# Performance work log

Measured on AMD Instinct MI355X. Metric: run time of the kernel, lower is better.

Reference implementation:

```python
import jax, jax.numpy as jnp
import numpy as np

DIM = 96
HEADS = 3
WIN = 7
HID = 384  # dim * mlp_ratio
EPS = 1e-5


def layernorm(x, w, b):
    mu = jnp.mean(x, axis=-1, keepdims=True)
    var = jnp.mean((x - mu) ** 2, axis=-1, keepdims=True)
    return (x - mu) * jax.lax.rsqrt(var + EPS) * w + b


def setup_inputs() -> dict:
    key = jax.random.key(0)
    ks = jax.random.split(key, 8)
    s = lambda n: 1.0 / np.sqrt(n)
    return {
        "x": jax.random.normal(ks[0], (8, DIM, 224, 224), dtype=jnp.float32),
        "norm1_w": jnp.ones((DIM,), jnp.float32),
        "norm1_b": jnp.zeros((DIM,), jnp.float32),
        "qkv_w": jax.random.normal(ks[1], (DIM, 3 * DIM), jnp.float32) * s(DIM),
        "qkv_b": jnp.zeros((3 * DIM,), jnp.float32),
        "proj_w": jax.random.normal(ks[2], (DIM, DIM), jnp.float32) * s(DIM),
        "proj_b": jnp.zeros((DIM,), jnp.float32),
        "norm2_w": jnp.ones((DIM,), jnp.float32),
        "norm2_b": jnp.zeros((DIM,), jnp.float32),
        "fc1_w": jax.random.normal(ks[3], (DIM, HID), jnp.float32) * s(DIM),
        "fc1_b": jnp.zeros((HID,), jnp.float32),
        "fc2_w": jax.random.normal(ks[4], (HID, DIM), jnp.float32) * s(HID),
        "fc2_b": jnp.zeros((DIM,), jnp.float32),
    }


def swin_block(x, norm1_w, norm1_b, qkv_w, qkv_b, proj_w, proj_b,
               norm2_w, norm2_b, fc1_w, fc1_b, fc2_w, fc2_b):
    B, C, H, W = x.shape
    hd = C // HEADS
    scale = hd ** -0.5
    N = WIN * WIN
    # [B, H*W, C]
    tok = jnp.transpose(x.reshape(B, C, H * W), (0, 2, 1))
    shortcut = tok
    t = layernorm(tok, norm1_w, norm1_b).reshape(B, H, W, C)
    nH, nW = H // WIN, W // WIN
    wins = t.reshape(B, nH, WIN, nW, WIN, C).transpose(0, 1, 3, 2, 4, 5)
    wins = wins.reshape(-1, N, C)  # [B*nH*nW, N, C]
    # window MHA
    qkv = (wins @ qkv_w + qkv_b).reshape(-1, N, 3, HEADS, hd)
    q, k, v = jnp.moveaxis(qkv, 2, 0)  # each [Bw, N, HEADS, hd]
    attn = jnp.einsum('bnhd,bmhd->bhnm', q, k) * scale
    attn = jax.nn.softmax(attn, axis=-1)
    o = jnp.einsum('bhnm,bmhd->bnhd', attn, v).reshape(-1, N, C)
    o = o @ proj_w + proj_b
    # window reverse
    o = o.reshape(B, nH, nW, WIN, WIN, C).transpose(0, 1, 3, 2, 4, 5)
    o = o.reshape(B, H * W, C)
    t = shortcut + o
    # MLP block
    m = layernorm(t, norm2_w, norm2_b)
    m = jax.nn.gelu(m @ fc1_w + fc1_b, approximate=False) @ fc2_w + fc2_b
    t = t + m
    return jnp.transpose(t, (0, 2, 1)).reshape(B, C, H, W)


def reference(x, norm1_w, norm1_b, qkv_w, qkv_b, proj_w, proj_b,
              norm2_w, norm2_b, fc1_w, fc1_b, fc2_w, fc2_b):
    return swin_block(x, norm1_w, norm1_b, qkv_w, qkv_b, proj_w, proj_b,
                      norm2_w, norm2_b, fc1_w, fc1_b, fc2_w, fc2_b)
```

## Files before the change

### kernel.cpp

```cpp
#include <hip/hip_runtime.h>


typedef __bf16 bf16;
typedef __attribute__((ext_vector_type(8))) __bf16 bf16x8;
typedef __attribute__((ext_vector_type(4))) float f32x4;
typedef __attribute__((ext_vector_type(4))) int i32x4;

#define LDA 104
#define LDV 72
#define LDW 233
#define TOKW 6144

union U8 { int i[4]; bf16x8 v; };

__device__ __forceinline__ f32x4 mfma16(bf16x8 a, bf16x8 b, f32x4 c) {
    return __builtin_amdgcn_mfma_f32_16x16x32_bf16(a, b, c, 0, 0, 0);
}
__device__ __forceinline__ int pkbf(float lo, float hi) {
    int r; asm("v_cvt_pk_bf16_f32 %0, %1, %2" : "=v"(r) : "v"(lo), "v"(hi)); return r;
}
__device__ __forceinline__ float rcpf(float x) {
    float r; asm("v_rcp_f32 %0, %1" : "=v"(r) : "v"(x)); return r;
}
__device__ __forceinline__ float gelu_f(float v) {
    const float a = -2.30220770f, b = -0.10294852f;
    float e = exp2f(v * __builtin_fmaf(b, v * v, a));
    return v * rcpf(1.f + e);
}

__global__ void swin_wprep(const float* __restrict__ qkv_w,
                           const float* __restrict__ proj_w,
                           const float* __restrict__ fc1_w,
                           const float* __restrict__ fc2_w,
                           bf16* __restrict__ wsT) {
    int i = blockIdx.x * 256 + threadIdx.x;
    if (i < 27648) { int n = i / 96, k = i - n * 96; wsT[i] = (bf16)qkv_w[k * 288 + n]; }
    else if (i < 36864) { int j = i - 27648, n = j / 96, k = j - n * 96; wsT[i] = (bf16)proj_w[k * 96 + n]; }
    else if (i < 73728) { int j = i - 36864, n = j / 96, k = j - n * 96; wsT[i] = (bf16)fc1_w[k * 384 + n]; }
    else if (i < 110592){ int j = i - 73728, n = j / 384, k = j - n * 384; wsT[i] = (bf16)fc2_w[k * 96 + n]; }
}

__global__ void swin_padfill(bf16* __restrict__ tokW) {
    int id = blockIdx.x * 256 + threadIdx.x;
    int win = id / 180, r = id - win * 180;
    int row = 49 + r / 12, c8 = r - (r / 12) * 12;
    *(i32x4*)(tokW + (size_t)win * TOKW + row * 96 + c8 * 8) = i32x4{0, 0, 0, 0};
}

__global__ __launch_bounds__(256)
void swin_gather(const float* __restrict__ x, bf16* __restrict__ tokW) {
    __shared__ bf16 sT[96 * LDW];
    const int tid = threadIdx.x;
    const int bi = blockIdx.x;
    const int b = bi / 224, h = bi - b * 224;
    const int wy = h / 7, ty = h - wy * 7;
    const size_t xbase = (size_t)b * 4816896 + (size_t)h * 224;

#pragma unroll
    for (int i = 0; i < 21; ++i) {
        int id = i * 256 + tid;
        int c = id / 56, w4 = id - c * 56;
        f32x4 v = *(const f32x4*)(x + xbase + (size_t)c * 50176 + w4 * 4);
#pragma unroll
        for (int j = 0; j < 4; ++j) sT[c * LDW + w4 * 4 + j] = (bf16)v[j];
    }
    __syncthreads();

#pragma unroll
    for (int i = 0; i < 11; ++i) {
        int id = i * 256 + tid;
        if (id < 2688) {
            int win = id / 84, r = id - win * 84;
            int tx = r / 12, c8 = r - tx * 12;
            bf16x8 v;
#pragma unroll
            for (int j = 0; j < 8; ++j) v[j] = sT[(c8 * 8 + j) * LDW + win * 7 + tx];
            *(i32x4*)(tokW + (size_t)(b * 1024 + wy * 32 + win) * TOKW
                      + (ty * 7 + tx) * 96 + c8 * 8) = *(i32x4*)&v;
        }
    }
}

__global__ __launch_bounds__(256)
void swin_scatter(const bf16* __restrict__ tokW, float* __restrict__ out) {
    __shared__ bf16 sT[96 * LDW];
    const int tid = threadIdx.x;
    const int bi = blockIdx.x;
    const int b = bi / 224, h = bi - b * 224;
    const int wy = h / 7, ty = h - wy * 7;
    const size_t obase = (size_t)b * 4816896 + (size_t)h * 224;

#pragma unroll
    for (int i = 0; i < 11; ++i) {
        int id = i * 256 + tid;
        if (id < 2688) {
            int win = id / 84, r = id - win * 84;
            int tx = r / 12, c8 = r - tx * 12;
            bf16x8 v = *(const bf16x8*)(tokW + (size_t)(b * 1024 + wy * 32 + win) * TOKW
                                        + (ty * 7 + tx) * 96 + c8 * 8);
#pragma unroll
            for (int j = 0; j < 8; ++j) sT[(c8 * 8 + j) * LDW + win * 7 + tx] = v[j];
        }
    }
    __syncthreads();

#pragma unroll
    for (int i = 0; i < 21; ++i) {
        int id = i * 256 + tid;
        int c = id / 56, w4 = id - c * 56;
        f32x4 v;
#pragma unroll
        for (int j = 0; j < 4; ++j) v[j] = (float)sT[c * LDW + w4 * 4 + j];
        *(f32x4*)(out + obase + (size_t)c * 50176 + w4 * 4) = v;
    }
}

__device__ __forceinline__ bf16x8 bload(const bf16* T, const float* worig,
                                        int nrow, int k0, int K, int N, bool wok) {
    if (wok) return *(const bf16x8*)(T + (size_t)nrow * K + k0);
    bf16x8 f;
#pragma unroll
    for (int j = 0; j < 8; ++j) f[j] = (bf16)worig[(size_t)(k0 + j) * N + nrow];
    return f;
}

__global__ __launch_bounds__(256, 4)
void swin_fused(const float* __restrict__ x, bf16* __restrict__ tokW,
                const float* __restrict__ n1w, const float* __restrict__ n1b,
                const float* __restrict__ qkvw, const float* __restrict__ qkvb,
                const float* __restrict__ projw, const float* __restrict__ projb,
                const float* __restrict__ n2w, const float* __restrict__ n2b,
                const float* __restrict__ fc1w, const float* __restrict__ fc1b,
                const float* __restrict__ fc2w, const float* __restrict__ fc2b,
                const bf16* __restrict__ wsT,
                float* __restrict__ out, int fast_i, int wok_i) {
    __shared__ __attribute__((aligned(16))) bf16 L[20224];
    bf16* RB = L;
    bf16* RC = L + 6656;
    bf16* RV = L + 13312;

    const bool fast = fast_i != 0;
    const bool wok  = wok_i != 0;

    const int tid  = threadIdx.x;
    const int wave = tid >> 6;
    const int lane = tid & 63;
    const int g    = lane >> 4;
    const int q16  = lane & 15;

    const int win = blockIdx.x;
    const int b  = win >> 10;
    const int wy = (win >> 5) & 31;
    const int wx = win & 31;
    const int h0 = wy * 7, w0 = wx * 7;
    const size_t xbase = (size_t)b * 4816896;
    const bf16* myWin = tokW + (size_t)win * TOKW;

    if (fast) {
#pragma unroll
        for (int i = 0; i < 3; ++i) {
            int id = i * 256 + tid;
            int row = id / 12, c8 = id - row * 12;
            *(i32x4*)&RB[row * LDA + c8 * 8] = *(const i32x4*)(myWin + row * 96 + c8 * 8);
        }
    } else {
        for (int i = 0; i < 24; ++i) {
            int id = i * 256 + tid;
            if (id < 4704) {
                int c = id / 49, pix = id - c * 49;
                int ty = pix / 7, tx = pix - ty * 7;
                RB[pix * LDA + c] =
                    (bf16)x[xbase + (size_t)c * 50176 + (h0 + ty) * 224 + w0 + tx];
            } else if (id < 6144) {
                int j = id - 4704;
                int row = 49 + j / 96, c = j - (j / 96) * 96;
                RB[row * LDA + c] = (bf16)0.f;
            }
        }
    }
    __syncthreads();

    {
        int r = tid >> 2, p = tid & 3;
        const int c0 = p * 24;
        bf16* rp = &RB[r * LDA + c0];
        bf16x8 v0 = *(const bf16x8*)rp;
        bf16x8 v1 = *(const bf16x8*)(rp + 8);
        bf16x8 v2 = *(const bf16x8*)(rp + 16);
        float s = 0.f, s2 = 0.f;
#pragma unroll
        for (int j = 0; j < 8; ++j) {
            float a = (float)v0[j], c = (float)v1[j], d = (float)v2[j];
            s += a + c + d; s2 += a * a + c * c + d * d;
        }
        s += __shfl_xor(s, 1);  s2 += __shfl_xor(s2, 1);
        s += __shfl_xor(s, 2);  s2 += __shfl_xor(s2, 2);
        float mu = s * (1.f / 96.f);
        float rs = rsqrtf(fmaxf(s2 * (1.f / 96.f) - mu * mu, 0.f) + 1e-5f);
        bf16x8 o0, o1, o2;
#pragma unroll
        for (int j = 0; j < 8; ++j) {
            o0[j] = (bf16)(((float)v0[j] - mu) * rs * n1w[c0 + j] + n1b[c0 + j]);
            o1[j] = (bf16)(((float)v1[j] - mu) * rs * n1w[c0 + 8 + j] + n1b[c0 + 8 + j]);
            o2[j] = (bf16)(((float)v2[j] - mu) * rs * n1w[c0 + 16 + j] + n1b[c0 + 16 + j]);
        }
        *(bf16x8*)rp = o0; *(bf16x8*)(rp + 8) = o1; *(bf16x8*)(rp + 16) = o2;
    }
    __syncthreads();

    bf16x8 afrag[3][4];
#pragma unroll
    for (int s = 0; s < 3; ++s)
#pragma unroll
        for (int m = 0; m < 4; ++m)
            afrag[s][m] = *(const bf16x8*)&RB[(m * 16 + q16) * LDA + s * 32 + g * 8];
    __syncthreads();

    const bf16* qkvT  = wsT;
    const bf16* projT = wsT + 27648;
    const bf16* fc1T  = wsT + 36864;
    const bf16* fc2T  = wsT + 73728;

    for (int nt = wave; nt < 18; nt += 4) {
        const int nrow = nt * 16 + q16;
        f32x4 acc[4] = {{0,0,0,0},{0,0,0,0},{0,0,0,0},{0,0,0,0}};
#pragma unroll
        for (int s = 0; s < 3; ++s) {
            bf16x8 bf = bload(qkvT, qkvw, nrow, s * 32 + g * 8, 96, 288, wok);
#pragma unroll
            for (int m = 0; m < 4; ++m) acc[m] = mfma16(afrag[s][m], bf, acc[m]);
        }
        float bias = qkvb[nrow];
#pragma unroll
        for (int m = 0; m < 4; ++m)
#pragma unroll
            for (int r = 0; r < 4; ++r) {
                float v = acc[m][r] + bias;
                int row = m * 16 + g * 4 + r;
                bf16 hv = (bf16)v;
                if (nrow < 96)        RB[row * LDA + nrow] = hv;
                else if (nrow < 192)  RC[row * LDA + (nrow - 96)] = hv;
                else                  RV[(nrow - 192) * LDV + row] = hv;
            }
    }
    __syncthreads();

    const float sc_l2e = 0.17677669529663688f * 1.4426950408889634f;
    const bool hi5 = (lane & 32) != 0;
    const int addr0 = ((lane & 16) << 3) | (q16 << 2);
    const int addr1 = addr0 + 64;
    f32x4 oacc[3][2];
#pragma unroll
    for (int h = 0; h < 3; ++h) {
        bf16x8 bq = *(const bf16x8*)&RB[(wave * 16 + q16) * LDA + h * 32 + g * 8];
        f32x4 s4s[4];
#pragma unroll
        for (int kt = 0; kt < 4; ++kt) {
            bf16x8 ak = *(const bf16x8*)&RC[(kt * 16 + q16) * LDA + h * 32 + g * 8];
            f32x4 z = {0, 0, 0, 0};
            s4s[kt] = mfma16(ak, bq, z);
        }
        float m0 = -1e30f;
#pragma unroll
        for (int kt = 0; kt < 3; ++kt)
#pragma unroll
            for (int r = 0; r < 4; ++r) m0 = fmaxf(m0, s4s[kt][r]);
        m0 = fmaxf(m0, (g == 0) ? s4s[3][0] : -1e30f);
        m0 = fmaxf(m0, __shfl_xor(m0, 16));
        m0 = fmaxf(m0, __shfl_xor(m0, 32));
        float ss = 0.f;
#pragma unroll
        for (int kt = 0; kt < 3; ++kt)
#pragma unroll
            for (int r = 0; r < 4; ++r) {
                float e = exp2f((s4s[kt][r] - m0) * sc_l2e);
                s4s[kt][r] = e; ss += e;
            }
        {
            float e = (g == 0) ? exp2f((s4s[3][0] - m0) * sc_l2e) : 0.f;
            s4s[3][0] = e; ss += e;
            s4s[3][1] = 0.f; s4s[3][2] = 0.f; s4s[3][3] = 0.f;
        }
        ss += __shfl_xor(ss, 16);
        ss += __shfl_xor(ss, 32);
        float inv = rcpf(ss);

        int u[4][2];
#pragma unroll
        for (int kt = 0; kt < 4; ++kt) {
            u[kt][0] = pkbf(s4s[kt][0], s4s[kt][1]);
            u[kt][1] = pkbf(s4s[kt][2], s4s[kt][3]);
        }
        bf16x8 ap[2];
#pragma unroll
        for (int kh = 0; kh < 2; ++kh) {
            U8 w;
            int a0 = __builtin_amdgcn_ds_bpermute(addr0, u[kh * 2][0]);
            int b0 = __builtin_amdgcn_ds_bpermute(addr0, u[kh * 2 + 1][0]);
            w.i[0] = hi5 ? b0 : a0;
            int a1 = __builtin_amdgcn_ds_bpermute(addr0, u[kh * 2][1]);
            int b1 = __builtin_amdgcn_ds_bpermute(addr0, u[kh * 2 + 1][1]);
            w.i[1] = hi5 ? b1 : a1;
            int a2 = __builtin_amdgcn_ds_bpermute(addr1, u[kh * 2][0]);
            int b2 = __builtin_amdgcn_ds_bpermute(addr1, u[kh * 2 + 1][0]);
            w.i[2] = hi5 ? b2 : a2;
            int a3 = __builtin_amdgcn_ds_bpermute(addr1, u[kh * 2][1]);
            int b3 = __builtin_amdgcn_ds_bpermute(addr1, u[kh * 2 + 1][1]);
            w.i[3] = hi5 ? b3 : a3;
            ap[kh] = w.v;
        }
#pragma unroll
        for (int n2 = 0; n2 < 2; ++n2) {
            int d0 = (h * 32 + n2 * 16 + q16) * LDV;
            f32x4 oa = {0, 0, 0, 0};
            oa = mfma16(*(const bf16x8*)&RV[d0 + g * 8], ap[0], oa);
            oa = mfma16(*(const bf16x8*)&RV[d0 + 32 + g * 8], ap[1], oa);
#pragma unroll
            for (int r = 0; r < 4; ++r) oa[r] *= inv;
            oacc[h][n2] = oa;
        }
    }
    __syncthreads();

    {
        int u2[3][2][2];
#pragma unroll
        for (int h = 0; h < 3; ++h)
#pragma unroll
            for (int n2 = 0; n2 < 2; ++n2) {
                u2[h][n2][0] = pkbf(oacc[h][n2][0], oacc[h][n2][1]);
                u2[h][n2][1] = pkbf(oacc[h][n2][2], oacc[h][n2][3]);
            }
        bf16x8 aoM[3];
#pragma unroll
        for (int s = 0; s < 3; ++s) {
            U8 w;
            int a0 = __builtin_amdgcn_ds_bpermute(addr0, u2[s][0][0]);
            int b0 = __builtin_amdgcn_ds_bpermute(addr0, u2[s][1][0]);
            w.i[0] = hi5 ? b0 : a0;
            int a1 = __builtin_amdgcn_ds_bpermute(addr0, u2[s][0][1]);
            int b1 = __builtin_amdgcn_ds_bpermute(addr0, u2[s][1][1]);
            w.i[1] = hi5 ? b1 : a1;
            int a2 = __builtin_amdgcn_ds_bpermute(addr1, u2[s][0][0]);
            int b2 = __builtin_amdgcn_ds_bpermute(addr1, u2[s][1][0]);
            w.i[2] = hi5 ? b2 : a2;
            int a3 = __builtin_amdgcn_ds_bpermute(addr1, u2[s][0][1]);
            int b3 = __builtin_amdgcn_ds_bpermute(addr1, u2[s][1][1]);
            w.i[3] = hi5 ? b3 : a3;
            aoM[s] = w.v;
        }
#pragma unroll
        for (int nt = 0; nt < 6; ++nt) {
            int nrow = nt * 16 + q16;
            f32x4 pacc = {0, 0, 0, 0};
#pragma unroll
            for (int s = 0; s < 3; ++s) {
                bf16x8 bf = bload(projT, projw, nrow, s * 32 + g * 8, 96, 96, wok);
                pacc = mfma16(aoM[s], bf, pacc);
            }
            float bias = projb[nrow];
#pragma unroll
            for (int r = 0; r < 4; ++r) {
                int row = wave * 16 + g * 4 + r;
                float sc;
                if (fast) sc = (float)myWin[row * 96 + nrow];
                else      sc = (row < 49)
                    ? x[xbase + (size_t)nrow * 50176 + (h0 + row / 7) * 224 + w0 + row % 7]
                    : 0.f;
                RV[row * LDA + nrow] = (bf16)(pacc[r] + bias + sc);
            }
        }
    }
    __syncthreads();

    {
        int r = tid >> 2, p = tid & 3;
        const int c0 = p * 24;
        const bf16* rp = &RV[r * LDA + c0];
        bf16x8 v0 = *(const bf16x8*)rp;
        bf16x8 v1 = *(const bf16x8*)(rp + 8);
        bf16x8 v2 = *(const bf16x8*)(rp + 16);
        float s = 0.f, s2 = 0.f;
#pragma unroll
        for (int j = 0; j < 8; ++j) {
            float a = (float)v0[j], c = (float)v1[j], d = (float)v2[j];
            s += a + c + d; s2 += a * a + c * c + d * d;
        }
        s += __shfl_xor(s, 1);  s2 += __shfl_xor(s2, 1);
        s += __shfl_xor(s, 2);  s2 += __shfl_xor(s2, 2);
        float mu = s * (1.f / 96.f);
        float rs = rsqrtf(fmaxf(s2 * (1.f / 96.f) - mu * mu, 0.f) + 1e-5f);
        bf16x8 o0, o1, o2;
#pragma unroll
        for (int j = 0; j < 8; ++j) {
            o0[j] = (bf16)(((float)v0[j] - mu) * rs * n2w[c0 + j] + n2b[c0 + j]);
            o1[j] = (bf16)(((float)v1[j] - mu) * rs * n2w[c0 + 8 + j] + n2b[c0 + 8 + j]);
            o2[j] = (bf16)(((float)v2[j] - mu) * rs * n2w[c0 + 16 + j] + n2b[c0 + 16 + j]);
        }
        bf16* wp = &RB[r * LDA + c0];
        *(bf16x8*)wp = o0; *(bf16x8*)(wp + 8) = o1; *(bf16x8*)(wp + 16) = o2;
    }
    __syncthreads();

    const int npt = (wave < 2) ? 2 : 1;
    f32x4 f2acc[2][4] = {{{0,0,0,0},{0,0,0,0},{0,0,0,0},{0,0,0,0}},
                         {{0,0,0,0},{0,0,0,0},{0,0,0,0},{0,0,0,0}}};
    for (int ch = 0; ch < 4; ++ch) {
#pragma unroll
        for (int t = 0; t < 2; ++t) {
            if (t < npt) {
                int ntl = (t == 0) ? wave : wave + 4;
                int nrow = (ch * 6 + ntl) * 16 + q16;
                f32x4 acc[4] = {{0,0,0,0},{0,0,0,0},{0,0,0,0},{0,0,0,0}};
#pragma unroll
                for (int s = 0; s < 3; ++s) {
                    bf16x8 bf = bload(fc1T, fc1w, nrow, s * 32 + g * 8, 96, 384, wok);
#pragma unroll
                    for (int m = 0; m < 4; ++m) {
                        bf16x8 a = *(const bf16x8*)&RB[(m * 16 + q16) * LDA + s * 32 + g * 8];
                        acc[m] = mfma16(a, bf, acc[m]);
                    }
                }
                float bias = fc1b[nrow];
#pragma unroll
                for (int m = 0; m < 4; ++m)
#pragma unroll
                    for (int r = 0; r < 4; ++r)
                        RC[(m * 16 + g * 4 + r) * LDA + ntl * 16 + q16] =
                            (bf16)gelu_f(acc[m][r] + bias);
            }
        }
        __syncthreads();
#pragma unroll
        for (int s = 0; s < 3; ++s) {
            bf16x8 a0 = *(const bf16x8*)&RC[(q16)      * LDA + s * 32 + g * 8];
            bf16x8 a1 = *(const bf16x8*)&RC[(16 + q16) * LDA + s * 32 + g * 8];
            bf16x8 a2 = *(const bf16x8*)&RC[(32 + q16) * LDA + s * 32 + g * 8];
            bf16x8 a3 = *(const bf16x8*)&RC[(48 + q16) * LDA + s * 32 + g * 8];
#pragma unroll
            for (int t = 0; t < 2; ++t) {
                if (t < npt) {
                    int nt = (t == 0) ? wave : wave + 4;
                    int nrow = nt * 16 + q16;
                    bf16x8 bf = bload(fc2T, fc2w, nrow, ch * 96 + s * 32 + g * 8, 384, 96, wok);
                    f2acc[t][0] = mfma16(a0, bf, f2acc[t][0]);
                    f2acc[t][1] = mfma16(a1, bf, f2acc[t][1]);
                    f2acc[t][2] = mfma16(a2, bf, f2acc[t][2]);
                    f2acc[t][3] = mfma16(a3, bf, f2acc[t][3]);
                }
            }
        }
        __syncthreads();
    }

#pragma unroll
    for (int t = 0; t < 2; ++t) {
        if (t < npt) {
            int col = ((t == 0) ? wave : wave + 4) * 16 + q16;
            float bias = fc2b[col];
#pragma unroll
            for (int m = 0; m < 4; ++m)
#pragma unroll
                for (int r = 0; r < 4; ++r) {
                    int row = m * 16 + g * 4 + r;
                    float t2 = (float)RV[row * LDA + col];
                    RV[row * LDA + col] = (bf16)(f2acc[t][m][r] + bias + t2);
                }
        }
    }
    __syncthreads();

    if (fast) {
#pragma unroll
        for (int i = 0; i < 3; ++i) {
            int id = i * 256 + tid;
            if (id < 588) {
                int row = id / 12, c8 = id - row * 12;
                *(i32x4*)(tokW + (size_t)win * TOKW + row * 96 + c8 * 8) =
                    *(const i32x4*)&RV[row * LDA + c8 * 8];
            }
        }
    } else {
        for (int i = 0; i < 19; ++i) {
            int id = i * 256 + tid;
            if (id < 4704) {
                int c = id / 49, pix = id - c * 49;
                int ty = pix / 7, tx = pix - ty * 7;
                out[xbase + (size_t)c * 50176 + (h0 + ty) * 224 + w0 + tx] =
                    (float)RV[pix * LDA + c];
            }
        }
    }
}

extern "C" void kernel_launch(void* const* d_in, const int* in_sizes, int n_in,
                              void* d_out, int out_size, void* d_ws, size_t ws_size,
                              hipStream_t stream) {
    const float* x      = (const float*)d_in[0];
    const float* n1w    = (const float*)d_in[1];
    const float* n1b    = (const float*)d_in[2];
    const float* qkv_w  = (const float*)d_in[3];
    const float* qkv_b  = (const float*)d_in[4];
    const float* proj_w = (const float*)d_in[5];
    const float* proj_b = (const float*)d_in[6];
    const float* n2w    = (const float*)d_in[7];
    const float* n2b    = (const float*)d_in[8];
    const float* fc1_w  = (const float*)d_in[9];
    const float* fc1_b  = (const float*)d_in[10];
    const float* fc2_w  = (const float*)d_in[11];
    const float* fc2_b  = (const float*)d_in[12];
    float* out = (float*)d_out;

    const size_t TOKW_OFF = 225280;
    const int wok  = (ws_size >= 221184) ? 1 : 0;
    const int fast = (ws_size >= TOKW_OFF + 100663296ull) ? 1 : 0;
    bf16* wsT  = (bf16*)d_ws;
    bf16* tokW = (bf16*)((char*)d_ws + TOKW_OFF);

    if (wok)
        swin_wprep<<<dim3(432), dim3(256), 0, stream>>>(qkv_w, proj_w, fc1_w, fc2_w, wsT);
    if (fast) {
        swin_padfill<<<dim3(5760), dim3(256), 0, stream>>>(tokW);
        swin_gather<<<dim3(1792), dim3(256), 0, stream>>>(x, tokW);
    }
    swin_fused<<<dim3(8192), dim3(256), 0, stream>>>(
        x, tokW, n1w, n1b, qkv_w, qkv_b, proj_w, proj_b, n2w, n2b,
        fc1_w, fc1_b, fc2_w, fc2_b, wsT, out, fast, wok);
    if (fast)
        swin_scatter<<<dim3(1792), dim3(256), 0, stream>>>(tokW, out);
}
```

Before: 444.5 us.

## Keep per-wave token rows in registers through proj, LayerNorm2 and MLP

Result: slower. 785.1 us (+76.6%).

```diff
diff --git a/kernel.cpp b/kernel.cpp
--- a/kernel.cpp
+++ b/kernel.cpp
@@ -26,6 +26,29 @@
     const float a = -2.30220770f, b = -0.10294852f;
     float e = exp2f(v * __builtin_fmaf(b, v * v, a));
     return v * rcpf(1.f + e);
+}
+__device__ __forceinline__ float bf2f(int dw, int hi) {
+    union { int i; float f; } u;
+    u.i = hi ? (dw & 0xffff0000) : (dw << 16);
+    return u.f;
+}
+
+__device__ __forceinline__ bf16x8 xp(int p0, int p1, int q0, int q1,
+                                     int addr0, int addr1, bool hi5) {
+    U8 w;
+    int a0 = __builtin_amdgcn_ds_bpermute(addr0, p0);
+    int b0 = __builtin_amdgcn_ds_bpermute(addr0, q0);
+    w.i[0] = hi5 ? b0 : a0;
+    int a1 = __builtin_amdgcn_ds_bpermute(addr0, p1);
+    int b1 = __builtin_amdgcn_ds_bpermute(addr0, q1);
+    w.i[1] = hi5 ? b1 : a1;
+    int a2 = __builtin_amdgcn_ds_bpermute(addr1, p0);
+    int b2 = __builtin_amdgcn_ds_bpermute(addr1, q0);
+    w.i[2] = hi5 ? b2 : a2;
+    int a3 = __builtin_amdgcn_ds_bpermute(addr1, p1);
+    int b3 = __builtin_amdgcn_ds_bpermute(addr1, q1);
+    w.i[3] = hi5 ? b3 : a3;
+    return w.v;
 }
 
 __global__ void swin_wprep(const float* __restrict__ qkv_w,
@@ -134,10 +157,9 @@
                 const float* __restrict__ fc2w, const float* __restrict__ fc2b,
                 const bf16* __restrict__ wsT,
                 float* __restrict__ out, int fast_i, int wok_i) {
-    __shared__ __attribute__((aligned(16))) bf16 L[20224];
+    __shared__ __attribute__((aligned(16))) bf16 L[13568];
     bf16* RB = L;
-    bf16* RC = L + 6656;
-    bf16* RV = L + 13312;
+    bf16* RV = L + 6656;
 
     const bool fast = fast_i != 0;
     const bool wok  = wok_i != 0;
@@ -155,6 +177,10 @@
     const int h0 = wy * 7, w0 = wx * 7;
     const size_t xbase = (size_t)b * 4816896;
     const bf16* myWin = tokW + (size_t)win * TOKW;
+
+    const bool hi5 = (lane & 32) != 0;
+    const int addr0 = ((lane & 16) << 3) | (q16 << 2);
+    const int addr1 = addr0 + 64;
 
     if (fast) {
 #pragma unroll
@@ -221,44 +247,69 @@
     const bf16* fc1T  = wsT + 36864;
     const bf16* fc2T  = wsT + 73728;
 
-    for (int nt = wave; nt < 18; nt += 4) {
-        const int nrow = nt * 16 + q16;
-        f32x4 acc[4] = {{0,0,0,0},{0,0,0,0},{0,0,0,0},{0,0,0,0}};
-#pragma unroll
-        for (int s = 0; s < 3; ++s) {
-            bf16x8 bf = bload(qkvT, qkvw, nrow, s * 32 + g * 8, 96, 288, wok);
-#pragma unroll
-            for (int m = 0; m < 4; ++m) acc[m] = mfma16(afrag[s][m], bf, acc[m]);
-        }
-        float bias = qkvb[nrow];
-#pragma unroll
-        for (int m = 0; m < 4; ++m)
-#pragma unroll
-            for (int r = 0; r < 4; ++r) {
-                float v = acc[m][r] + bias;
-                int row = m * 16 + g * 4 + r;
-                bf16 hv = (bf16)v;
-                if (nrow < 96)        RB[row * LDA + nrow] = hv;
-                else if (nrow < 192)  RC[row * LDA + (nrow - 96)] = hv;
-                else                  RV[(nrow - 192) * LDV + row] = hv;
-            }
+    bf16x8 bq[3];
+    {
+        int uq[6][2];
+#pragma unroll
+        for (int nt = 0; nt < 6; ++nt) {
+            f32x4 qa = {0, 0, 0, 0};
+#pragma unroll
+            for (int s = 0; s < 3; ++s)
+                qa = mfma16(bload(qkvT, qkvw, nt * 16 + q16, s * 32 + g * 8, 96, 288, wok),
+                            afrag[s][wave], qa);
+            f32x4 qb = *(const f32x4*)(qkvb + nt * 16 + g * 4);
+            uq[nt][0] = pkbf(qa[0] + qb[0], qa[1] + qb[1]);
+            uq[nt][1] = pkbf(qa[2] + qb[2], qa[3] + qb[3]);
+        }
+#pragma unroll
+        for (int h = 0; h < 3; ++h)
+            bq[h] = xp(uq[2 * h][0], uq[2 * h][1], uq[2 * h + 1][0], uq[2 * h + 1][1],
+                       addr0, addr1, hi5);
+    }
+
+    {
+        const int base = 6 + wave * 3;
+#pragma unroll
+        for (int i = 0; i < 3; ++i) {
+            const int nt = base + i;
+            const int nrow = nt * 16 + q16;
+            f32x4 acc[4] = {{0,0,0,0},{0,0,0,0},{0,0,0,0},{0,0,0,0}};
+#pragma unroll
+            for (int s = 0; s < 3; ++s) {
+                bf16x8 bf = bload(qkvT, qkvw, nrow, s * 32 + g * 8, 96, 288, wok);
+#pragma unroll
+                for (int m = 0; m < 4; ++m) acc[m] = mfma16(afrag[s][m], bf, acc[m]);
+            }
+            float bias = qkvb[nrow];
+            if (wave < 2) {
+#pragma unroll
+                for (int m = 0; m < 4; ++m)
+#pragma unroll
+                    for (int r = 0; r < 4; ++r)
+                        RB[(m * 16 + g * 4 + r) * LDA + (nt - 6) * 16 + q16] =
+                            (bf16)(acc[m][r] + bias);
+            } else {
+#pragma unroll
+                for (int m = 0; m < 4; ++m)
+#pragma unroll
+                    for (int r = 0; r < 4; ++r)
+                        RV[((nt - 12) * 16 + q16) * LDV + m * 16 + g * 4 + r] =
+                            (bf16)(acc[m][r] + bias);
+            }
+        }
     }
     __syncthreads();
 
     const float sc_l2e = 0.17677669529663688f * 1.4426950408889634f;
-    const bool hi5 = (lane & 32) != 0;
-    const int addr0 = ((lane & 16) << 3) | (q16 << 2);
-    const int addr1 = addr0 + 64;
     f32x4 oacc[3][2];
 #pragma unroll
     for (int h = 0; h < 3; ++h) {
-        bf16x8 bq = *(const bf16x8*)&RB[(wave * 16 + q16) * LDA + h * 32 + g * 8];
         f32x4 s4s[4];
 #pragma unroll
         for (int kt = 0; kt < 4; ++kt) {
-            bf16x8 ak = *(const bf16x8*)&RC[(kt * 16 + q16) * LDA + h * 32 + g * 8];
+            bf16x8 ak = *(const bf16x8*)&RB[(kt * 16 + q16) * LDA + h * 32 + g * 8];
             f32x4 z = {0, 0, 0, 0};
-            s4s[kt] = mfma16(ak, bq, z);
+            s4s[kt] = mfma16(ak, bq[h], z);
         }
         float m0 = -1e30f;
 #pragma unroll
@@ -291,181 +342,128 @@
             u[kt][0] = pkbf(s4s[kt][0], s4s[kt][1]);
             u[kt][1] = pkbf(s4s[kt][2], s4s[kt][3]);
         }
-        bf16x8 ap[2];
-#pragma unroll
-        for (int kh = 0; kh < 2; ++kh) {
-            U8 w;
-            int a0 = __builtin_amdgcn_ds_bpermute(addr0, u[kh * 2][0]);
-            int b0 = __builtin_amdgcn_ds_bpermute(addr0, u[kh * 2 + 1][0]);
-            w.i[0] = hi5 ? b0 : a0;
-            int a1 = __builtin_amdgcn_ds_bpermute(addr0, u[kh * 2][1]);
-            int b1 = __builtin_amdgcn_ds_bpermute(addr0, u[kh * 2 + 1][1]);
-            w.i[1] = hi5 ? b1 : a1;
-            int a2 = __builtin_amdgcn_ds_bpermute(addr1, u[kh * 2][0]);
-            int b2 = __builtin_amdgcn_ds_bpermute(addr1, u[kh * 2 + 1][0]);
-            w.i[2] = hi5 ? b2 : a2;
-            int a3 = __builtin_amdgcn_ds_bpermute(addr1, u[kh * 2][1]);
-            int b3 = __builtin_amdgcn_ds_bpermute(addr1, u[kh * 2 + 1][1]);
-            w.i[3] = hi5 ? b3 : a3;
-            ap[kh] = w.v;
-        }
+        bf16x8 ap0 = xp(u[0][0], u[0][1], u[1][0], u[1][1], addr0, addr1, hi5);
+        bf16x8 ap1 = xp(u[2][0], u[2][1], u[3][0], u[3][1], addr0, addr1, hi5);
 #pragma unroll
         for (int n2 = 0; n2 < 2; ++n2) {
             int d0 = (h * 32 + n2 * 16 + q16) * LDV;
             f32x4 oa = {0, 0, 0, 0};
-            oa = mfma16(*(const bf16x8*)&RV[d0 + g * 8], ap[0], oa);
-            oa = mfma16(*(const bf16x8*)&RV[d0 + 32 + g * 8], ap[1], oa);
+            oa = mfma16(*(const bf16x8*)&RV[d0 + g * 8], ap0, oa);
+            oa = mfma16(*(const bf16x8*)&RV[d0 + 32 + g * 8], ap1, oa);
 #pragma unroll
             for (int r = 0; r < 4; ++r) oa[r] *= inv;
             oacc[h][n2] = oa;
         }
     }
-    __syncthreads();
-
+
+    float t2f[6][4];
     {
-        int u2[3][2][2];
+        int uo[3][2][2];
 #pragma unroll
         for (int h = 0; h < 3; ++h)
 #pragma unroll
             for (int n2 = 0; n2 < 2; ++n2) {
-                u2[h][n2][0] = pkbf(oacc[h][n2][0], oacc[h][n2][1]);
-                u2[h][n2][1] = pkbf(oacc[h][n2][2], oacc[h][n2][3]);
+                uo[h][n2][0] = pkbf(oacc[h][n2][0], oacc[h][n2][1]);
+                uo[h][n2][1] = pkbf(oacc[h][n2][2], oacc[h][n2][3]);
             }
         bf16x8 aoM[3];
 #pragma unroll
-        for (int s = 0; s < 3; ++s) {
-            U8 w;
-            int a0 = __builtin_amdgcn_ds_bpermute(addr0, u2[s][0][0]);
-            int b0 = __builtin_amdgcn_ds_bpermute(addr0, u2[s][1][0]);
-            w.i[0] = hi5 ? b0 : a0;
-            int a1 = __builtin_amdgcn_ds_bpermute(addr0, u2[s][0][1]);
-            int b1 = __builtin_amdgcn_ds_bpermute(addr0, u2[s][1][1]);
-            w.i[1] = hi5 ? b1 : a1;
-            int a2 = __builtin_amdgcn_ds_bpermute(addr1, u2[s][0][0]);
-            int b2 = __builtin_amdgcn_ds_bpermute(addr1, u2[s][1][0]);
-            w.i[2] = hi5 ? b2 : a2;
-            int a3 = __builtin_amdgcn_ds_bpermute(addr1, u2[s][0][1]);
-            int b3 = __builtin_amdgcn_ds_bpermute(addr1, u2[s][1][1]);
-            w.i[3] = hi5 ? b3 : a3;
-            aoM[s] = w.v;
-        }
+        for (int s = 0; s < 3; ++s)
+            aoM[s] = xp(uo[s][0][0], uo[s][0][1], uo[s][1][0], uo[s][1][1],
+                        addr0, addr1, hi5);
+        const int tok = wave * 16 + q16;
 #pragma unroll
         for (int nt = 0; nt < 6; ++nt) {
-            int nrow = nt * 16 + q16;
-            f32x4 pacc = {0, 0, 0, 0};
-#pragma unroll
-            for (int s = 0; s < 3; ++s) {
-                bf16x8 bf = bload(projT, projw, nrow, s * 32 + g * 8, 96, 96, wok);
-                pacc = mfma16(aoM[s], bf, pacc);
-            }
-            float bias = projb[nrow];
+            f32x4 pa = {0, 0, 0, 0};
+#pragma unroll
+            for (int s = 0; s < 3; ++s)
+                pa = mfma16(bload(projT, projw, nt * 16 + q16, s * 32 + g * 8, 96, 96, wok),
+                            aoM[s], pa);
+            f32x4 pb = *(const f32x4*)(projb + nt * 16 + g * 4);
 #pragma unroll
             for (int r = 0; r < 4; ++r) {
-                int row = wave * 16 + g * 4 + r;
+                int dim = nt * 16 + g * 4 + r;
                 float sc;
-                if (fast) sc = (float)myWin[row * 96 + nrow];
-                else      sc = (row < 49)
-                    ? x[xbase + (size_t)nrow * 50176 + (h0 + row / 7) * 224 + w0 + row % 7]
+                if (fast) sc = (float)myWin[tok * 96 + dim];
+                else      sc = (tok < 49)
+                    ? x[xbase + (size_t)dim * 50176 + (h0 + tok / 7) * 224 + w0 + tok % 7]
                     : 0.f;
-                RV[row * LDA + nrow] = (bf16)(pacc[r] + bias + sc);
-            }
-        }
-    }
-    __syncthreads();
-
+                t2f[nt][r] = pa[r] + pb[r] + sc;
+            }
+        }
+    }
+
+    int u3[6][2], tr[6][2];
     {
-        int r = tid >> 2, p = tid & 3;
-        const int c0 = p * 24;
-        const bf16* rp = &RV[r * LDA + c0];
-        bf16x8 v0 = *(const bf16x8*)rp;
-        bf16x8 v1 = *(const bf16x8*)(rp + 8);
-        bf16x8 v2 = *(const bf16x8*)(rp + 16);
         float s = 0.f, s2 = 0.f;
 #pragma unroll
-        for (int j = 0; j < 8; ++j) {
-            float a = (float)v0[j], c = (float)v1[j], d = (float)v2[j];
-            s += a + c + d; s2 += a * a + c * c + d * d;
-        }
-        s += __shfl_xor(s, 1);  s2 += __shfl_xor(s2, 1);
-        s += __shfl_xor(s, 2);  s2 += __shfl_xor(s2, 2);
+        for (int nt = 0; nt < 6; ++nt)
+#pragma unroll
+            for (int r = 0; r < 4; ++r) { float v = t2f[nt][r]; s += v; s2 += v * v; }
+        s += __shfl_xor(s, 16);  s2 += __shfl_xor(s2, 16);
+        s += __shfl_xor(s, 32);  s2 += __shfl_xor(s2, 32);
         float mu = s * (1.f / 96.f);
         float rs = rsqrtf(fmaxf(s2 * (1.f / 96.f) - mu * mu, 0.f) + 1e-5f);
-        bf16x8 o0, o1, o2;
-#pragma unroll
-        for (int j = 0; j < 8; ++j) {
-            o0[j] = (bf16)(((float)v0[j] - mu) * rs * n2w[c0 + j] + n2b[c0 + j]);
-            o1[j] = (bf16)(((float)v1[j] - mu) * rs * n2w[c0 + 8 + j] + n2b[c0 + 8 + j]);
-            o2[j] = (bf16)(((float)v2[j] - mu) * rs * n2w[c0 + 16 + j] + n2b[c0 + 16 + j]);
-        }
-        bf16* wp = &RB[r * LDA + c0];
-        *(bf16x8*)wp = o0; *(bf16x8*)(wp + 8) = o1; *(bf16x8*)(wp + 16) = o2;
-    }
-    __syncthreads();
-
-    const int npt = (wave < 2) ? 2 : 1;
-    f32x4 f2acc[2][4] = {{{0,0,0,0},{0,0,0,0},{0,0,0,0},{0,0,0,0}},
-                         {{0,0,0,0},{0,0,0,0},{0,0,0,0},{0,0,0,0}}};
-    for (int ch = 0; ch < 4; ++ch) {
-#pragma unroll
-        for (int t = 0; t < 2; ++t) {
-            if (t < npt) {
-                int ntl = (t == 0) ? wave : wave + 4;
-                int nrow = (ch * 6 + ntl) * 16 + q16;
-                f32x4 acc[4] = {{0,0,0,0},{0,0,0,0},{0,0,0,0},{0,0,0,0}};
-#pragma unroll
-                for (int s = 0; s < 3; ++s) {
-                    bf16x8 bf = bload(fc1T, fc1w, nrow, s * 32 + g * 8, 96, 384, wok);
-#pragma unroll
-                    for (int m = 0; m < 4; ++m) {
-                        bf16x8 a = *(const bf16x8*)&RB[(m * 16 + q16) * LDA + s * 32 + g * 8];
-                        acc[m] = mfma16(a, bf, acc[m]);
-                    }
-                }
-                float bias = fc1b[nrow];
-#pragma unroll
-                for (int m = 0; m < 4; ++m)
-#pragma unroll
-                    for (int r = 0; r < 4; ++r)
-                        RC[(m * 16 + g * 4 + r) * LDA + ntl * 16 + q16] =
-                            (bf16)gelu_f(acc[m][r] + bias);
-            }
-        }
-        __syncthreads();
-#pragma unroll
-        for (int s = 0; s < 3; ++s) {
-            bf16x8 a0 = *(const bf16x8*)&RC[(q16)      * LDA + s * 32 + g * 8];
-            bf16x8 a1 = *(const bf16x8*)&RC[(16 + q16) * LDA + s * 32 + g * 8];
-            bf16x8 a2 = *(const bf16x8*)&RC[(32 + q16) * LDA + s * 32 + g * 8];
-            bf16x8 a3 = *(const bf16x8*)&RC[(48 + q16) * LDA + s * 32 + g * 8];
-#pragma unroll
-            for (int t = 0; t < 2; ++t) {
-                if (t < npt) {
-                    int nt = (t == 0) ? wave : wave + 4;
-                    int nrow = nt * 16 + q16;
-                    bf16x8 bf = bload(fc2T, fc2w, nrow, ch * 96 + s * 32 + g * 8, 384, 96, wok);
-                    f2acc[t][0] = mfma16(a0, bf, f2acc[t][0]);
-                    f2acc[t][1] = mfma16(a1, bf, f2acc[t][1]);
-                    f2acc[t][2] = mfma16(a2, bf, f2acc[t][2]);
-                    f2acc[t][3] = mfma16(a3, bf, f2acc[t][3]);
-                }
-            }
-        }
-        __syncthreads();
-    }
-
-#pragma unroll
-    for (int t = 0; t < 2; ++t) {
-        if (t < npt) {
-            int col = ((t == 0) ? wave : wave + 4) * 16 + q16;
-            float bias = fc2b[col];
-#pragma unroll
-            for (int m = 0; m < 4; ++m)
-#pragma unroll
-                for (int r = 0; r < 4; ++r) {
-                    int row = m * 16 + g * 4 + r;
-                    float t2 = (float)RV[row * LDA + col];
-                    RV[row * LDA + col] = (bf16)(f2acc[t][m][r] + bias + t2);
-                }
+#pragma unroll
+        for (int nt = 0; nt < 6; ++nt) {
+            f32x4 nw = *(const f32x4*)(n2w + nt * 16 + g * 4);
+            f32x4 nb = *(const f32x4*)(n2b + nt * 16 + g * 4);
+            float tn[4];
+#pragma unroll
+            for (int r = 0; r < 4; ++r)
+                tn[r] = (t2f[nt][r] - mu) * rs * nw[r] + nb[r];
+            u3[nt][0] = pkbf(tn[0], tn[1]);
+            u3[nt][1] = pkbf(tn[2], tn[3]);
+            tr[nt][0] = pkbf(t2f[nt][0], t2f[nt][1]);
+            tr[nt][1] = pkbf(t2f[nt][2], t2f[nt][3]);
+        }
+    }
+    bf16x8 bt2n[3];
+#pragma unroll
+    for (int s = 0; s < 3; ++s)
+        bt2n[s] = xp(u3[2 * s][0], u3[2 * s][1], u3[2 * s + 1][0], u3[2 * s + 1][1],
+                     addr0, addr1, hi5);
+
+    f32x4 facc[6] = {{0,0,0,0},{0,0,0,0},{0,0,0,0},{0,0,0,0},{0,0,0,0},{0,0,0,0}};
+    for (int ch = 0; ch < 6; ++ch) {
+        int u4[4][2];
+#pragma unroll
+        for (int t4 = 0; t4 < 4; ++t4) {
+            f32x4 ha = {0, 0, 0, 0};
+#pragma unroll
+            for (int s = 0; s < 3; ++s)
+                ha = mfma16(bload(fc1T, fc1w, ch * 64 + t4 * 16 + q16,
+                                  s * 32 + g * 8, 96, 384, wok),
+                            bt2n[s], ha);
+            f32x4 hb = *(const f32x4*)(fc1b + ch * 64 + t4 * 16 + g * 4);
+            float hg[4];
+#pragma unroll
+            for (int r = 0; r < 4; ++r) hg[r] = gelu_f(ha[r] + hb[r]);
+            u4[t4][0] = pkbf(hg[0], hg[1]);
+            u4[t4][1] = pkbf(hg[2], hg[3]);
+        }
+        bf16x8 bh0 = xp(u4[0][0], u4[0][1], u4[1][0], u4[1][1], addr0, addr1, hi5);
+        bf16x8 bh1 = xp(u4[2][0], u4[2][1], u4[3][0], u4[3][1], addr0, addr1, hi5);
+#pragma unroll
+        for (int nt = 0; nt < 6; ++nt) {
+            facc[nt] = mfma16(bload(fc2T, fc2w, nt * 16 + q16,
+                                    ch * 64 + g * 8, 384, 96, wok), bh0, facc[nt]);
+            facc[nt] = mfma16(bload(fc2T, fc2w, nt * 16 + q16,
+                                    ch * 64 + 32 + g * 8, 384, 96, wok), bh1, facc[nt]);
+        }
+    }
+
+    __syncthreads();
+    {
+        const int tok = wave * 16 + q16;
+#pragma unroll
+        for (int nt = 0; nt < 6; ++nt) {
+            f32x4 fb = *(const f32x4*)(fc2b + nt * 16 + g * 4);
+#pragma unroll
+            for (int r = 0; r < 4; ++r) {
+                float v = facc[nt][r] + fb[r] + bf2f(tr[nt][r >> 1], r & 1);
+                RB[tok * LDA + nt * 16 + g * 4 + r] = (bf16)v;
+            }
         }
     }
     __syncthreads();
@@ -477,7 +475,7 @@
             if (id < 588) {
                 int row = id / 12, c8 = id - row * 12;
                 *(i32x4*)(tokW + (size_t)win * TOKW + row * 96 + c8 * 8) =
-                    *(const i32x4*)&RV[row * LDA + c8 * 8];
+                    *(const i32x4*)&RB[row * LDA + c8 * 8];
             }
         }
     } else {
@@ -487,7 +485,7 @@
                 int c = id / 49, pix = id - c * 49;
                 int ty = pix / 7, tx = pix - ty * 7;
                 out[xbase + (size_t)c * 50176 + (h0 + ty) * 224 + w0 + tx] =
-                    (float)RV[pix * LDA + c];
+                    (float)RB[pix * LDA + c];
             }
         }
     }
```
